# Optimization experiments

Measured on AMD Instinct MI355X. Metric: run time of the kernel, lower is better.

The kernel has to match this reference:

```python
import jax, jax.numpy as jnp
import numpy as np

N_NODES = 100000
HID = 128
N_EDGES = 600000


def sage_conv(h, src, dst, Wl, bl, Wr, n_nodes):
    # PyG SAGEConv (mean aggr): out = lin_l(mean_{j->i} h_j) + lin_r(h_i)
    msgs = h[src]                                               # [E, d] gather
    agg = jax.ops.segment_sum(msgs, dst, num_segments=n_nodes)  # [N, d]
    cnt = jax.ops.segment_sum(jnp.ones((src.shape[0], 1), h.dtype), dst,
                              num_segments=n_nodes)             # [N, 1]
    mean = agg / jnp.maximum(cnt, 1.0)                          # isolated nodes -> 0
    return mean @ Wl.T + bl + h @ Wr.T


def setup_inputs() -> dict:
    key = jax.random.key(0)
    ks = jax.random.split(key, 8)
    scale = 1.0 / np.sqrt(HID)
    x = jnp.arange(N_NODES, dtype=jnp.int64) if jax.config.jax_enable_x64 else jnp.arange(N_NODES, dtype=jnp.int32)
    edge_index = jax.random.randint(ks[0], (2, N_EDGES), 0, N_NODES)
    emb = jax.random.normal(ks[1], (N_NODES, HID), dtype=jnp.float32) * scale
    Wl1 = jax.random.normal(ks[2], (HID, HID), dtype=jnp.float32) * scale
    bl1 = jnp.zeros((HID,), jnp.float32)
    Wr1 = jax.random.normal(ks[3], (HID, HID), dtype=jnp.float32) * scale
    Wl2 = jax.random.normal(ks[4], (HID, HID), dtype=jnp.float32) * scale
    bl2 = jnp.zeros((HID,), jnp.float32)
    Wr2 = jax.random.normal(ks[5], (HID, HID), dtype=jnp.float32) * scale
    return {"x": x, "edge_index": edge_index, "emb": emb,
            "Wl1": Wl1, "bl1": bl1, "Wr1": Wr1,
            "Wl2": Wl2, "bl2": bl2, "Wr2": Wr2}


def reference(x, edge_index, emb, Wl1, bl1, Wr1, Wl2, bl2, Wr2):
    src, dst = edge_index[0], edge_index[1]
    n = emb.shape[0]
    h = emb[x]                                          # embedding lookup [N, d]
    h = jax.nn.relu(sage_conv(h, src, dst, Wl1, bl1, Wr1, n))  # dropout = eval identity
    h = jax.nn.relu(sage_conv(h, src, dst, Wl2, bl2, Wr2, n))
    return h
```

## Files before the change

kernel.cpp:

```cpp
#include <hip/hip_runtime.h>

#define HID 128

typedef unsigned short ushort_t;
typedef unsigned int uint_t;
typedef float f32x4 __attribute__((ext_vector_type(4)));
typedef short s16x8 __attribute__((ext_vector_type(8)));

__device__ __forceinline__ ushort_t f2bf(float f) {
  uint_t u = __float_as_uint(f);
  uint_t r = (u + 0x7FFFu + ((u >> 16) & 1u)) >> 16;
  return (ushort_t)r;
}
__device__ __forceinline__ float bfLo(uint_t v) { return __uint_as_float(v << 16); }
__device__ __forceinline__ float bfHi(uint_t v) { return __uint_as_float(v & 0xFFFF0000u); }

__global__ __launch_bounds__(256) void prep_kernel(
    const float* __restrict__ emb, const int* __restrict__ x,
    ushort_t* __restrict__ hb, int N,
    const float* __restrict__ Wl1, const float* __restrict__ Wr1,
    const float* __restrict__ Wl2, const float* __restrict__ Wr2,
    ushort_t* __restrict__ wsw,
    const int* __restrict__ dst, int* __restrict__ deg, int E) {
  int tid = blockIdx.x * 256 + threadIdx.x;
  const int halfN = (N + 1) >> 1;
  int gthreads = halfN * 16;
  if (tid < gthreads) {
    int r0 = tid >> 4, j = (tid & 15) * 8;
    int r1 = r0 + halfN;
    int s0 = x[r0];
    int s1 = (r1 < N) ? x[r1] : s0;
    const float* src0 = &emb[(size_t)s0 * HID + j];
    const float* src1 = &emb[(size_t)s1 * HID + j];
    float4 a0 = *(const float4*)src0;
    float4 a1 = *(const float4*)(src0 + 4);
    float4 b0 = *(const float4*)src1;
    float4 b1 = *(const float4*)(src1 + 4);
    uint4 p;
    p.x = (uint_t)f2bf(a0.x) | ((uint_t)f2bf(a0.y) << 16);
    p.y = (uint_t)f2bf(a0.z) | ((uint_t)f2bf(a0.w) << 16);
    p.z = (uint_t)f2bf(a1.x) | ((uint_t)f2bf(a1.y) << 16);
    p.w = (uint_t)f2bf(a1.z) | ((uint_t)f2bf(a1.w) << 16);
    *(uint4*)&hb[(size_t)r0 * HID + j] = p;
    if (r1 < N) {
      uint4 q;
      q.x = (uint_t)f2bf(b0.x) | ((uint_t)f2bf(b0.y) << 16);
      q.y = (uint_t)f2bf(b0.z) | ((uint_t)f2bf(b0.w) << 16);
      q.z = (uint_t)f2bf(b1.x) | ((uint_t)f2bf(b1.y) << 16);
      q.w = (uint_t)f2bf(b1.z) | ((uint_t)f2bf(b1.w) << 16);
      *(uint4*)&hb[(size_t)r1 * HID + j] = q;
    }
    return;
  }
  tid -= gthreads;
  if (tid < 65536) {
    const float* srcs[4] = {Wl1, Wr1, Wl2, Wr2};
    int m = tid >> 14, idx = tid & 16383;
    int j = idx & 7;
    int lane = (idx >> 3) & 63;
    int nt = (idx >> 9) & 7;
    int ks = (idx >> 12) & 3;
    int row = nt * 16 + (lane & 15);
    int col = ks * 32 + (lane >> 4) * 8 + j;
    wsw[tid] = f2bf(srcs[m][row * HID + col]);
    return;
  }
  tid -= 65536;
  if (tid < E) atomicAdd(&deg[dst[tid]], 1);
}

__global__ __launch_bounds__(256) void scan1_kernel(
    const int* __restrict__ deg, int* __restrict__ offsets,
    int* __restrict__ sums, int N) {
  __shared__ int s[256];
  int b = blockIdx.x, t = threadIdx.x;
  int base = b * 1024 + t * 4;
  int v0 = 0, v1 = 0, v2 = 0, v3 = 0;
  if (base + 0 < N) v0 = deg[base + 0];
  if (base + 1 < N) v1 = deg[base + 1];
  if (base + 2 < N) v2 = deg[base + 2];
  if (base + 3 < N) v3 = deg[base + 3];
  int mySum = v0 + v1 + v2 + v3;
  s[t] = mySum;
  __syncthreads();
  for (int off = 1; off < 256; off <<= 1) {
    int v = (t >= off) ? s[t - off] : 0;
    __syncthreads();
    s[t] += v;
    __syncthreads();
  }
  int excl = s[t] - mySum;
  if (t == 255) sums[b] = s[255];
  if (base + 0 < N) offsets[base + 0] = excl;
  if (base + 1 < N) offsets[base + 1] = excl + v0;
  if (base + 2 < N) offsets[base + 2] = excl + v0 + v1;
  if (base + 3 < N) offsets[base + 3] = excl + v0 + v1 + v2;
}

__global__ __launch_bounds__(256) void scan3_kernel(
    int* __restrict__ offsets, const int* __restrict__ sums,
    int* __restrict__ cursor, int N, int E, int nb) {
  __shared__ int red[256];
  int t = threadIdx.x;
  int chunk = (blockIdx.x * 256) >> 10;
  red[t] = (t < chunk) ? sums[t] : 0;
  __syncthreads();
  for (int off = 128; off > 0; off >>= 1) {
    if (t < off) red[t] += red[t + off];
    __syncthreads();
  }
  int prefix = red[0];
  int i = blockIdx.x * 256 + t;
  if (i < N) {
    int v = offsets[i] + prefix;
    offsets[i] = v;
    cursor[i] = v;
  } else if (i == N) {
    offsets[N] = E;
  }
}

__global__ __launch_bounds__(256) void fill_kernel(
    const int* __restrict__ src, const int* __restrict__ dst,
    int* __restrict__ cursor, int* __restrict__ csr, int E) {
  int e = blockIdx.x * 256 + threadIdx.x;
  if (e >= E) return;
  int d = dst[e];
  int pos = atomicAdd(&cursor[d], 1);
  csr[pos] = src[e];
}

__global__ __launch_bounds__(256) void aggregate_kernel(
    const ushort_t* __restrict__ hb, const int* __restrict__ offsets,
    const int* __restrict__ csr, ushort_t* __restrict__ meanb, int N) {
  int t = threadIdx.x;
  int node = blockIdx.x * 16 + (t >> 4);
  if (node >= N) return;
  int l15 = t & 15;
  int o0 = offsets[node], o1 = offsets[node + 1];

  float acc[8];
#pragma unroll
  for (int i = 0; i < 8; i++) acc[i] = 0.f;

  int e = o0;
  for (; e + 3 < o1; e += 4) {
    int s0 = csr[e], s1 = csr[e + 1], s2 = csr[e + 2], s3 = csr[e + 3];
    uint4 v0 = *(const uint4*)&hb[(size_t)s0 * HID + l15 * 8];
    uint4 v1 = *(const uint4*)&hb[(size_t)s1 * HID + l15 * 8];
    uint4 v2 = *(const uint4*)&hb[(size_t)s2 * HID + l15 * 8];
    uint4 v3 = *(const uint4*)&hb[(size_t)s3 * HID + l15 * 8];
    acc[0] += (bfLo(v0.x) + bfLo(v1.x)) + (bfLo(v2.x) + bfLo(v3.x));
    acc[1] += (bfHi(v0.x) + bfHi(v1.x)) + (bfHi(v2.x) + bfHi(v3.x));
    acc[2] += (bfLo(v0.y) + bfLo(v1.y)) + (bfLo(v2.y) + bfLo(v3.y));
    acc[3] += (bfHi(v0.y) + bfHi(v1.y)) + (bfHi(v2.y) + bfHi(v3.y));
    acc[4] += (bfLo(v0.z) + bfLo(v1.z)) + (bfLo(v2.z) + bfLo(v3.z));
    acc[5] += (bfHi(v0.z) + bfHi(v1.z)) + (bfHi(v2.z) + bfHi(v3.z));
    acc[6] += (bfLo(v0.w) + bfLo(v1.w)) + (bfLo(v2.w) + bfLo(v3.w));
    acc[7] += (bfHi(v0.w) + bfHi(v1.w)) + (bfHi(v2.w) + bfHi(v3.w));
  }
  if (e + 1 < o1) {
    int s0 = csr[e], s1 = csr[e + 1];
    uint4 v0 = *(const uint4*)&hb[(size_t)s0 * HID + l15 * 8];
    uint4 v1 = *(const uint4*)&hb[(size_t)s1 * HID + l15 * 8];
    acc[0] += bfLo(v0.x) + bfLo(v1.x);
    acc[1] += bfHi(v0.x) + bfHi(v1.x);
    acc[2] += bfLo(v0.y) + bfLo(v1.y);
    acc[3] += bfHi(v0.y) + bfHi(v1.y);
    acc[4] += bfLo(v0.z) + bfLo(v1.z);
    acc[5] += bfHi(v0.z) + bfHi(v1.z);
    acc[6] += bfLo(v0.w) + bfLo(v1.w);
    acc[7] += bfHi(v0.w) + bfHi(v1.w);
    e += 2;
  }
  if (e < o1) {
    int s0 = csr[e];
    uint4 v0 = *(const uint4*)&hb[(size_t)s0 * HID + l15 * 8];
    acc[0] += bfLo(v0.x); acc[1] += bfHi(v0.x);
    acc[2] += bfLo(v0.y); acc[3] += bfHi(v0.y);
    acc[4] += bfLo(v0.z); acc[5] += bfHi(v0.z);
    acc[6] += bfLo(v0.w); acc[7] += bfHi(v0.w);
  }

  int d = o1 - o0;
  float inv = 1.0f / (float)(d > 1 ? d : 1);
  uint4 p;
  p.x = (uint_t)f2bf(acc[0] * inv) | ((uint_t)f2bf(acc[1] * inv) << 16);
  p.y = (uint_t)f2bf(acc[2] * inv) | ((uint_t)f2bf(acc[3] * inv) << 16);
  p.z = (uint_t)f2bf(acc[4] * inv) | ((uint_t)f2bf(acc[5] * inv) << 16);
  p.w = (uint_t)f2bf(acc[6] * inv) | ((uint_t)f2bf(acc[7] * inv) << 16);
  *(uint4*)&meanb[(size_t)node * HID + l15 * 8] = p;
}

__global__ __launch_bounds__(256) void mfma_gemm_kernel(
    const ushort_t* __restrict__ meanb, const ushort_t* __restrict__ hb,
    const ushort_t* __restrict__ WlS, const ushort_t* __restrict__ WrS,
    const float* __restrict__ bias, float* __restrict__ outF,
    ushort_t* __restrict__ outB, int N, int outIsBf16) {
  __shared__ ushort_t ws[32768];
  const int t = threadIdx.x;
  const int wave = t >> 6;
  const int lane = t & 63;
  const int rowBase = (blockIdx.x * 4 + wave) * 32;
  const int l15 = lane & 15;
  const int quad = lane >> 4;
  const int kq = quad * 8;
  const bool active = rowBase < N;

  int r0 = rowBase + l15;       if (r0 >= N) r0 = N - 1;
  int r1 = rowBase + 16 + l15;  if (r1 >= N) r1 = N - 1;

  s16x8 a[2][2][4];
  if (active) {
#pragma unroll
    for (int ks = 0; ks < 4; ks++) {
      a[0][0][ks] = *(const s16x8*)&meanb[(size_t)r0 * HID + ks * 32 + kq];
      a[0][1][ks] = *(const s16x8*)&meanb[(size_t)r1 * HID + ks * 32 + kq];
      a[1][0][ks] = *(const s16x8*)&hb[(size_t)r0 * HID + ks * 32 + kq];
      a[1][1][ks] = *(const s16x8*)&hb[(size_t)r1 * HID + ks * 32 + kq];
    }
  }

#pragma unroll
  for (int it = 0; it < 8; it++) {
    int o = (it * 256 + t) * 8;
    *(s16x8*)&ws[o] = *(const s16x8*)&WlS[o];
    *(s16x8*)&ws[16384 + o] = *(const s16x8*)&WrS[o];
  }
  __syncthreads();

  if (active) {
    f32x4 acc[2][8];
#pragma unroll
    for (int mt = 0; mt < 2; mt++)
#pragma unroll
      for (int nt = 0; nt < 8; nt++) acc[mt][nt] = (f32x4){0.f, 0.f, 0.f, 0.f};

#pragma unroll
    for (int half = 0; half < 2; half++) {
      const int hbase = half * 16384;
#pragma unroll
      for (int ks = 0; ks < 4; ks++)
#pragma unroll
        for (int nt = 0; nt < 8; nt++) {
          s16x8 b = *(const s16x8*)&ws[hbase + ((ks * 8 + nt) * 64 + lane) * 8];
          acc[0][nt] = __builtin_amdgcn_mfma_f32_16x16x32_bf16(a[half][0][ks], b, acc[0][nt], 0, 0, 0);
          acc[1][nt] = __builtin_amdgcn_mfma_f32_16x16x32_bf16(a[half][1][ks], b, acc[1][nt], 0, 0, 0);
        }
    }

#pragma unroll
    for (int mt = 0; mt < 2; mt++) {
#pragma unroll
      for (int nt = 0; nt < 8; nt++) {
        int col = nt * 16 + l15;
        float bv = bias[col];
#pragma unroll
        for (int r = 0; r < 4; r++) {
          int row = rowBase + mt * 16 + quad * 4 + r;
          if (row < N) {
            float v = fmaxf(acc[mt][nt][r] + bv, 0.f);
            if (outIsBf16) outB[(size_t)row * HID + col] = f2bf(v);
            else           outF[(size_t)row * HID + col] = v;
          }
        }
      }
    }
  }
}

extern "C" void kernel_launch(void* const* d_in, const int* in_sizes, int n_in,
                              void* d_out, int out_size, void* d_ws, size_t ws_size,
                              hipStream_t stream) {
  const int* x = (const int*)d_in[0];
  const int* ei = (const int*)d_in[1];
  const float* emb = (const float*)d_in[2];
  const float* Wl1 = (const float*)d_in[3];
  const float* bl1 = (const float*)d_in[4];
  const float* Wr1 = (const float*)d_in[5];
  const float* Wl2 = (const float*)d_in[6];
  const float* bl2 = (const float*)d_in[7];
  const float* Wr2 = (const float*)d_in[8];
  float* out = (float*)d_out;

  const int N = in_sizes[0];
  const int E = in_sizes[1] / 2;
  const int* srcI = ei;
  const int* dstI = ei + E;

  char* p = (char*)d_ws;
  ushort_t* hb = (ushort_t*)p;    p += (size_t)N * HID * sizeof(ushort_t);
  ushort_t* meanb = (ushort_t*)p; p += (size_t)N * HID * sizeof(ushort_t);
  ushort_t* wb = (ushort_t*)p;    p += (size_t)4 * 16384 * sizeof(ushort_t);
  int* deg = (int*)p;             p += (size_t)((N + 3) & ~3) * sizeof(int);
  int* offsets = (int*)p;         p += (size_t)((N + 4) & ~3) * sizeof(int);
  int* cursor = (int*)p;          p += (size_t)((N + 3) & ~3) * sizeof(int);
  int* csr = (int*)p;             p += (size_t)((E + 3) & ~3) * sizeof(int);
  int* sums = (int*)p;            p += 256 * sizeof(int);

  ushort_t* Wlb1 = wb;
  ushort_t* Wrb1 = wb + 16384;
  ushort_t* Wlb2 = wb + 32768;
  ushort_t* Wrb2 = wb + 49152;

  const int nScanBlocks = (N + 1023) / 1024;
  const int eBlocks = (E + 255) / 256;
  const int gemmBlocks = (N + 127) / 128;
  const int aggBlocks = (N + 15) / 16;
  const int halfN = (N + 1) / 2;
  const int prepBlocks = (halfN * 16 + 65536 + E + 255) / 256;

  hipMemsetAsync(deg, 0, (size_t)N * sizeof(int), stream);
  prep_kernel<<<prepBlocks, 256, 0, stream>>>(emb, x, hb, N,
                                              Wl1, Wr1, Wl2, Wr2, wb,
                                              dstI, deg, E);
  scan1_kernel<<<nScanBlocks, 256, 0, stream>>>(deg, offsets, sums, N);
  scan3_kernel<<<(N + 256) / 256, 256, 0, stream>>>(offsets, sums, cursor,
                                                    N, E, nScanBlocks);
  fill_kernel<<<eBlocks, 256, 0, stream>>>(srcI, dstI, cursor, csr, E);

  aggregate_kernel<<<aggBlocks, 256, 0, stream>>>(hb, offsets, csr, meanb, N);
  mfma_gemm_kernel<<<gemmBlocks, 256, 0, stream>>>(meanb, hb, Wlb1, Wrb1, bl1,
                                                   nullptr, hb, N, 1);

  aggregate_kernel<<<aggBlocks, 256, 0, stream>>>(hb, offsets, csr, meanb, N);
  mfma_gemm_kernel<<<gemmBlocks, 256, 0, stream>>>(meanb, hb, Wlb2, Wrb2, bl2,
                                                   out, nullptr, N, 0);
}
```

Measured before the change: 293.6 us.

## Fuse mean aggregation with MFMA GEMM per layer via LDS mean tile

Merges the aggregate and GEMM kernels into one per-layer kernel. Each block gathers neighbour means for its 128 rows into a padded LDS tile and feeds them straight to the MFMA loop, removing the global round trip of the mean buffer and one launch per layer. Weights are now staged in quarter-size LDS chunks with extra barriers so the mean tile fits, and ping-pong hb buffers avoid read/write hazards. The prep kernel also handles four embedding rows per thread instead of two.

```diff
diff --git a/kernel.cpp b/kernel.cpp
--- a/kernel.cpp
+++ b/kernel.cpp
@@ -1,6 +1,7 @@
 #include <hip/hip_runtime.h>
 
 #define HID 128
+#define MEAN_STRIDE 136
 
 typedef unsigned short ushort_t;
 typedef unsigned int uint_t;
@@ -14,6 +15,15 @@
 }
 __device__ __forceinline__ float bfLo(uint_t v) { return __uint_as_float(v << 16); }
 __device__ __forceinline__ float bfHi(uint_t v) { return __uint_as_float(v & 0xFFFF0000u); }
+
+__device__ __forceinline__ uint4 pack8(const float4& lo, const float4& hi) {
+  uint4 p;
+  p.x = (uint_t)f2bf(lo.x) | ((uint_t)f2bf(lo.y) << 16);
+  p.y = (uint_t)f2bf(lo.z) | ((uint_t)f2bf(lo.w) << 16);
+  p.z = (uint_t)f2bf(hi.x) | ((uint_t)f2bf(hi.y) << 16);
+  p.w = (uint_t)f2bf(hi.z) | ((uint_t)f2bf(hi.w) << 16);
+  return p;
+}
 
 __global__ __launch_bounds__(256) void prep_kernel(
     const float* __restrict__ emb, const int* __restrict__ x,
@@ -23,33 +33,27 @@
     ushort_t* __restrict__ wsw,
     const int* __restrict__ dst, int* __restrict__ deg, int E) {
   int tid = blockIdx.x * 256 + threadIdx.x;
-  const int halfN = (N + 1) >> 1;
-  int gthreads = halfN * 16;
+  const int qN = (N + 3) >> 2;
+  int gthreads = qN * 16;
   if (tid < gthreads) {
     int r0 = tid >> 4, j = (tid & 15) * 8;
-    int r1 = r0 + halfN;
+    int r1 = r0 + qN, r2 = r0 + 2 * qN, r3 = r0 + 3 * qN;
     int s0 = x[r0];
     int s1 = (r1 < N) ? x[r1] : s0;
-    const float* src0 = &emb[(size_t)s0 * HID + j];
-    const float* src1 = &emb[(size_t)s1 * HID + j];
-    float4 a0 = *(const float4*)src0;
-    float4 a1 = *(const float4*)(src0 + 4);
-    float4 b0 = *(const float4*)src1;
-    float4 b1 = *(const float4*)(src1 + 4);
-    uint4 p;
-    p.x = (uint_t)f2bf(a0.x) | ((uint_t)f2bf(a0.y) << 16);
-    p.y = (uint_t)f2bf(a0.z) | ((uint_t)f2bf(a0.w) << 16);
-    p.z = (uint_t)f2bf(a1.x) | ((uint_t)f2bf(a1.y) << 16);
-    p.w = (uint_t)f2bf(a1.z) | ((uint_t)f2bf(a1.w) << 16);
-    *(uint4*)&hb[(size_t)r0 * HID + j] = p;
-    if (r1 < N) {
-      uint4 q;
-      q.x = (uint_t)f2bf(b0.x) | ((uint_t)f2bf(b0.y) << 16);
-      q.y = (uint_t)f2bf(b0.z) | ((uint_t)f2bf(b0.w) << 16);
-      q.z = (uint_t)f2bf(b1.x) | ((uint_t)f2bf(b1.y) << 16);
-      q.w = (uint_t)f2bf(b1.z) | ((uint_t)f2bf(b1.w) << 16);
-      *(uint4*)&hb[(size_t)r1 * HID + j] = q;
-    }
+    int s2 = (r2 < N) ? x[r2] : s0;
+    int s3 = (r3 < N) ? x[r3] : s0;
+    const float* p0 = &emb[(size_t)s0 * HID + j];
+    const float* p1 = &emb[(size_t)s1 * HID + j];
+    const float* p2 = &emb[(size_t)s2 * HID + j];
+    const float* p3 = &emb[(size_t)s3 * HID + j];
+    float4 a0 = *(const float4*)p0, a1 = *(const float4*)(p0 + 4);
+    float4 b0 = *(const float4*)p1, b1 = *(const float4*)(p1 + 4);
+    float4 c0 = *(const float4*)p2, c1 = *(const float4*)(p2 + 4);
+    float4 d0 = *(const float4*)p3, d1 = *(const float4*)(p3 + 4);
+    *(uint4*)&hb[(size_t)r0 * HID + j] = pack8(a0, a1);
+    if (r1 < N) *(uint4*)&hb[(size_t)r1 * HID + j] = pack8(b0, b1);
+    if (r2 < N) *(uint4*)&hb[(size_t)r2 * HID + j] = pack8(c0, c1);
+    if (r3 < N) *(uint4*)&hb[(size_t)r3 * HID + j] = pack8(d0, d1);
     return;
   }
   tid -= gthreads;
@@ -130,125 +134,150 @@
   csr[pos] = src[e];
 }
 
-__global__ __launch_bounds__(256) void aggregate_kernel(
-    const ushort_t* __restrict__ hb, const int* __restrict__ offsets,
-    const int* __restrict__ csr, ushort_t* __restrict__ meanb, int N) {
-  int t = threadIdx.x;
-  int node = blockIdx.x * 16 + (t >> 4);
-  if (node >= N) return;
-  int l15 = t & 15;
-  int o0 = offsets[node], o1 = offsets[node + 1];
-
-  float acc[8];
-#pragma unroll
-  for (int i = 0; i < 8; i++) acc[i] = 0.f;
-
-  int e = o0;
-  for (; e + 3 < o1; e += 4) {
-    int s0 = csr[e], s1 = csr[e + 1], s2 = csr[e + 2], s3 = csr[e + 3];
-    uint4 v0 = *(const uint4*)&hb[(size_t)s0 * HID + l15 * 8];
-    uint4 v1 = *(const uint4*)&hb[(size_t)s1 * HID + l15 * 8];
-    uint4 v2 = *(const uint4*)&hb[(size_t)s2 * HID + l15 * 8];
-    uint4 v3 = *(const uint4*)&hb[(size_t)s3 * HID + l15 * 8];
-    acc[0] += (bfLo(v0.x) + bfLo(v1.x)) + (bfLo(v2.x) + bfLo(v3.x));
-    acc[1] += (bfHi(v0.x) + bfHi(v1.x)) + (bfHi(v2.x) + bfHi(v3.x));
-    acc[2] += (bfLo(v0.y) + bfLo(v1.y)) + (bfLo(v2.y) + bfLo(v3.y));
-    acc[3] += (bfHi(v0.y) + bfHi(v1.y)) + (bfHi(v2.y) + bfHi(v3.y));
-    acc[4] += (bfLo(v0.z) + bfLo(v1.z)) + (bfLo(v2.z) + bfLo(v3.z));
-    acc[5] += (bfHi(v0.z) + bfHi(v1.z)) + (bfHi(v2.z) + bfHi(v3.z));
-    acc[6] += (bfLo(v0.w) + bfLo(v1.w)) + (bfLo(v2.w) + bfLo(v3.w));
-    acc[7] += (bfHi(v0.w) + bfHi(v1.w)) + (bfHi(v2.w) + bfHi(v3.w));
-  }
-  if (e + 1 < o1) {
-    int s0 = csr[e], s1 = csr[e + 1];
-    uint4 v0 = *(const uint4*)&hb[(size_t)s0 * HID + l15 * 8];
-    uint4 v1 = *(const uint4*)&hb[(size_t)s1 * HID + l15 * 8];
-    acc[0] += bfLo(v0.x) + bfLo(v1.x);
-    acc[1] += bfHi(v0.x) + bfHi(v1.x);
-    acc[2] += bfLo(v0.y) + bfLo(v1.y);
-    acc[3] += bfHi(v0.y) + bfHi(v1.y);
-    acc[4] += bfLo(v0.z) + bfLo(v1.z);
-    acc[5] += bfHi(v0.z) + bfHi(v1.z);
-    acc[6] += bfLo(v0.w) + bfLo(v1.w);
-    acc[7] += bfHi(v0.w) + bfHi(v1.w);
-    e += 2;
-  }
-  if (e < o1) {
-    int s0 = csr[e];
-    uint4 v0 = *(const uint4*)&hb[(size_t)s0 * HID + l15 * 8];
-    acc[0] += bfLo(v0.x); acc[1] += bfHi(v0.x);
-    acc[2] += bfLo(v0.y); acc[3] += bfHi(v0.y);
-    acc[4] += bfLo(v0.z); acc[5] += bfHi(v0.z);
-    acc[6] += bfLo(v0.w); acc[7] += bfHi(v0.w);
-  }
-
-  int d = o1 - o0;
-  float inv = 1.0f / (float)(d > 1 ? d : 1);
-  uint4 p;
-  p.x = (uint_t)f2bf(acc[0] * inv) | ((uint_t)f2bf(acc[1] * inv) << 16);
-  p.y = (uint_t)f2bf(acc[2] * inv) | ((uint_t)f2bf(acc[3] * inv) << 16);
-  p.z = (uint_t)f2bf(acc[4] * inv) | ((uint_t)f2bf(acc[5] * inv) << 16);
-  p.w = (uint_t)f2bf(acc[6] * inv) | ((uint_t)f2bf(acc[7] * inv) << 16);
-  *(uint4*)&meanb[(size_t)node * HID + l15 * 8] = p;
-}
-
-__global__ __launch_bounds__(256) void mfma_gemm_kernel(
-    const ushort_t* __restrict__ meanb, const ushort_t* __restrict__ hb,
+__global__ __launch_bounds__(256, 3) void fused_layer_kernel(
+    const ushort_t* __restrict__ hbIn,
+    const int* __restrict__ offsets, const int* __restrict__ csr,
     const ushort_t* __restrict__ WlS, const ushort_t* __restrict__ WrS,
-    const float* __restrict__ bias, float* __restrict__ outF,
-    ushort_t* __restrict__ outB, int N, int outIsBf16) {
-  __shared__ ushort_t ws[32768];
+    const float* __restrict__ bias,
+    float* __restrict__ outF, ushort_t* __restrict__ outB,
+    int N, int outIsBf16) {
+  __shared__ ushort_t lmean[128 * MEAN_STRIDE];
+  __shared__ ushort_t ws[8192];
   const int t = threadIdx.x;
+  const int lane = t & 63;
   const int wave = t >> 6;
-  const int lane = t & 63;
-  const int rowBase = (blockIdx.x * 4 + wave) * 32;
   const int l15 = lane & 15;
   const int quad = lane >> 4;
   const int kq = quad * 8;
-  const bool active = rowBase < N;
-
-  int r0 = rowBase + l15;       if (r0 >= N) r0 = N - 1;
-  int r1 = rowBase + 16 + l15;  if (r1 >= N) r1 = N - 1;
-
-  s16x8 a[2][2][4];
+  const int blockRow = blockIdx.x * 128;
+  const int waveRow = blockRow + wave * 32;
+  const bool active = waveRow < N;
+
+  int r0 = waveRow + l15;      if (r0 >= N) r0 = N - 1;
+  int r1 = waveRow + 16 + l15; if (r1 >= N) r1 = N - 1;
+  s16x8 ah0[4], ah1[4];
+#pragma unroll
+  for (int ks = 0; ks < 4; ks++) {
+    ah0[ks] = *(const s16x8*)&hbIn[(size_t)r0 * HID + ks * 32 + kq];
+    ah1[ks] = *(const s16x8*)&hbIn[(size_t)r1 * HID + ks * 32 + kq];
+  }
+
+  const int qw = t >> 4;
+#pragma unroll 1
+  for (int i = 0; i < 8; i++) {
+    int rl = qw * 8 + i;
+    int node = blockRow + rl;
+    uint4 p;
+    p.x = p.y = p.z = p.w = 0u;
+    if (node < N) {
+      int o0 = offsets[node], o1 = offsets[node + 1];
+      float acc[8];
+#pragma unroll
+      for (int q = 0; q < 8; q++) acc[q] = 0.f;
+      int e = o0;
+      for (; e + 3 < o1; e += 4) {
+        int s0 = csr[e], s1 = csr[e + 1], s2 = csr[e + 2], s3 = csr[e + 3];
+        uint4 v0 = *(const uint4*)&hbIn[(size_t)s0 * HID + l15 * 8];
+        uint4 v1 = *(const uint4*)&hbIn[(size_t)s1 * HID + l15 * 8];
+        uint4 v2 = *(const uint4*)&hbIn[(size_t)s2 * HID + l15 * 8];
+        uint4 v3 = *(const uint4*)&hbIn[(size_t)s3 * HID + l15 * 8];
+        acc[0] += (bfLo(v0.x) + bfLo(v1.x)) + (bfLo(v2.x) + bfLo(v3.x));
+        acc[1] += (bfHi(v0.x) + bfHi(v1.x)) + (bfHi(v2.x) + bfHi(v3.x));
+        acc[2] += (bfLo(v0.y) + bfLo(v1.y)) + (bfLo(v2.y) + bfLo(v3.y));
+        acc[3] += (bfHi(v0.y) + bfHi(v1.y)) + (bfHi(v2.y) + bfHi(v3.y));
+        acc[4] += (bfLo(v0.z) + bfLo(v1.z)) + (bfLo(v2.z) + bfLo(v3.z));
+        acc[5] += (bfHi(v0.z) + bfHi(v1.z)) + (bfHi(v2.z) + bfHi(v3.z));
+        acc[6] += (bfLo(v0.w) + bfLo(v1.w)) + (bfLo(v2.w) + bfLo(v3.w));
+        acc[7] += (bfHi(v0.w) + bfHi(v1.w)) + (bfHi(v2.w) + bfHi(v3.w));
+      }
+      if (e + 1 < o1) {
+        int s0 = csr[e], s1 = csr[e + 1];
+        uint4 v0 = *(const uint4*)&hbIn[(size_t)s0 * HID + l15 * 8];
+        uint4 v1 = *(const uint4*)&hbIn[(size_t)s1 * HID + l15 * 8];
+        acc[0] += bfLo(v0.x) + bfLo(v1.x);
+        acc[1] += bfHi(v0.x) + bfHi(v1.x);
+        acc[2] += bfLo(v0.y) + bfLo(v1.y);
+        acc[3] += bfHi(v0.y) + bfHi(v1.y);
+        acc[4] += bfLo(v0.z) + bfLo(v1.z);
+        acc[5] += bfHi(v0.z) + bfHi(v1.z);
+        acc[6] += bfLo(v0.w) + bfLo(v1.w);
+        acc[7] += bfHi(v0.w) + bfHi(v1.w);
+        e += 2;
+      }
+      if (e < o1) {
+        int s0 = csr[e];
+        uint4 v0 = *(const uint4*)&hbIn[(size_t)s0 * HID + l15 * 8];
+        acc[0] += bfLo(v0.x); acc[1] += bfHi(v0.x);
+        acc[2] += bfLo(v0.y); acc[3] += bfHi(v0.y);
+        acc[4] += bfLo(v0.z); acc[5] += bfHi(v0.z);
+        acc[6] += bfLo(v0.w); acc[7] += bfHi(v0.w);
+      }
+      int d = o1 - o0;
+      float inv = 1.0f / (float)(d > 1 ? d : 1);
+      p.x = (uint_t)f2bf(acc[0] * inv) | ((uint_t)f2bf(acc[1] * inv) << 16);
+      p.y = (uint_t)f2bf(acc[2] * inv) | ((uint_t)f2bf(acc[3] * inv) << 16);
+      p.z = (uint_t)f2bf(acc[4] * inv) | ((uint_t)f2bf(acc[5] * inv) << 16);
+      p.w = (uint_t)f2bf(acc[6] * inv) | ((uint_t)f2bf(acc[7] * inv) << 16);
+    }
+    *(uint4*)&lmean[rl * MEAN_STRIDE + l15 * 8] = p;
+  }
+  __syncthreads();
+
+  f32x4 acc[2][8];
+#pragma unroll
+  for (int mt = 0; mt < 2; mt++)
+#pragma unroll
+    for (int nt = 0; nt < 8; nt++) acc[mt][nt] = (f32x4){0.f, 0.f, 0.f, 0.f};
+
+#pragma unroll
+  for (int kp = 0; kp < 2; kp++) {
+#pragma unroll
+    for (int it = 0; it < 4; it++) {
+      int o = (it * 256 + t) * 8;
+      *(s16x8*)&ws[o] = *(const s16x8*)&WlS[kp * 8192 + o];
+    }
+    __syncthreads();
+    if (active) {
+#pragma unroll
+      for (int ks2 = 0; ks2 < 2; ks2++) {
+        int ksg = kp * 2 + ks2;
+        s16x8 a0 = *(const s16x8*)&lmean[(wave * 32 + l15) * MEAN_STRIDE + ksg * 32 + kq];
+        s16x8 a1 = *(const s16x8*)&lmean[(wave * 32 + 16 + l15) * MEAN_STRIDE + ksg * 32 + kq];
+#pragma unroll
+        for (int nt = 0; nt < 8; nt++) {
+          s16x8 b = *(const s16x8*)&ws[((ks2 * 8 + nt) * 64 + lane) * 8];
+          acc[0][nt] = __builtin_amdgcn_mfma_f32_16x16x32_bf16(a0, b, acc[0][nt], 0, 0, 0);
+          acc[1][nt] = __builtin_amdgcn_mfma_f32_16x16x32_bf16(a1, b, acc[1][nt], 0, 0, 0);
+        }
+      }
+    }
+    __syncthreads();
+  }
+
+#pragma unroll
+  for (int kp = 0; kp < 2; kp++) {
+#pragma unroll
+    for (int it = 0; it < 4; it++) {
+      int o = (it * 256 + t) * 8;
+      *(s16x8*)&ws[o] = *(const s16x8*)&WrS[kp * 8192 + o];
+    }
+    __syncthreads();
+    if (active) {
+#pragma unroll
+      for (int ks2 = 0; ks2 < 2; ks2++) {
+        int ksg = kp * 2 + ks2;
+#pragma unroll
+        for (int nt = 0; nt < 8; nt++) {
+          s16x8 b = *(const s16x8*)&ws[((ks2 * 8 + nt) * 64 + lane) * 8];
+          acc[0][nt] = __builtin_amdgcn_mfma_f32_16x16x32_bf16(ah0[ksg], b, acc[0][nt], 0, 0, 0);
+          acc[1][nt] = __builtin_amdgcn_mfma_f32_16x16x32_bf16(ah1[ksg], b, acc[1][nt], 0, 0, 0);
+        }
+      }
+    }
+    __syncthreads();
+  }
+
   if (active) {
-#pragma unroll
-    for (int ks = 0; ks < 4; ks++) {
-      a[0][0][ks] = *(const s16x8*)&meanb[(size_t)r0 * HID + ks * 32 + kq];
-      a[0][1][ks] = *(const s16x8*)&meanb[(size_t)r1 * HID + ks * 32 + kq];
-      a[1][0][ks] = *(const s16x8*)&hb[(size_t)r0 * HID + ks * 32 + kq];
-      a[1][1][ks] = *(const s16x8*)&hb[(size_t)r1 * HID + ks * 32 + kq];
-    }
-  }
-
-#pragma unroll
-  for (int it = 0; it < 8; it++) {
-    int o = (it * 256 + t) * 8;
-    *(s16x8*)&ws[o] = *(const s16x8*)&WlS[o];
-    *(s16x8*)&ws[16384 + o] = *(const s16x8*)&WrS[o];
-  }
-  __syncthreads();
-
-  if (active) {
-    f32x4 acc[2][8];
-#pragma unroll
-    for (int mt = 0; mt < 2; mt++)
-#pragma unroll
-      for (int nt = 0; nt < 8; nt++) acc[mt][nt] = (f32x4){0.f, 0.f, 0.f, 0.f};
-
-#pragma unroll
-    for (int half = 0; half < 2; half++) {
-      const int hbase = half * 16384;
-#pragma unroll
-      for (int ks = 0; ks < 4; ks++)
-#pragma unroll
-        for (int nt = 0; nt < 8; nt++) {
-          s16x8 b = *(const s16x8*)&ws[hbase + ((ks * 8 + nt) * 64 + lane) * 8];
-          acc[0][nt] = __builtin_amdgcn_mfma_f32_16x16x32_bf16(a[half][0][ks], b, acc[0][nt], 0, 0, 0);
-          acc[1][nt] = __builtin_amdgcn_mfma_f32_16x16x32_bf16(a[half][1][ks], b, acc[1][nt], 0, 0, 0);
-        }
-    }
-
 #pragma unroll
     for (int mt = 0; mt < 2; mt++) {
 #pragma unroll
@@ -257,7 +286,7 @@
         float bv = bias[col];
 #pragma unroll
         for (int r = 0; r < 4; r++) {
-          int row = rowBase + mt * 16 + quad * 4 + r;
+          int row = waveRow + mt * 16 + quad * 4 + r;
           if (row < N) {
             float v = fmaxf(acc[mt][nt][r] + bv, 0.f);
             if (outIsBf16) outB[(size_t)row * HID + col] = f2bf(v);
@@ -290,7 +319,7 @@
 
   char* p = (char*)d_ws;
   ushort_t* hb = (ushort_t*)p;    p += (size_t)N * HID * sizeof(ushort_t);
-  ushort_t* meanb = (ushort_t*)p; p += (size_t)N * HID * sizeof(ushort_t);
+  ushort_t* hb2 = (ushort_t*)p;   p += (size_t)N * HID * sizeof(ushort_t);
   ushort_t* wb = (ushort_t*)p;    p += (size_t)4 * 16384 * sizeof(ushort_t);
   int* deg = (int*)p;             p += (size_t)((N + 3) & ~3) * sizeof(int);
   int* offsets = (int*)p;         p += (size_t)((N + 4) & ~3) * sizeof(int);
@@ -306,9 +335,8 @@
   const int nScanBlocks = (N + 1023) / 1024;
   const int eBlocks = (E + 255) / 256;
   const int gemmBlocks = (N + 127) / 128;
-  const int aggBlocks = (N + 15) / 16;
-  const int halfN = (N + 1) / 2;
-  const int prepBlocks = (halfN * 16 + 65536 + E + 255) / 256;
+  const int qN = (N + 3) / 4;
+  const int prepBlocks = (qN * 16 + 65536 + E + 255) / 256;
 
   hipMemsetAsync(deg, 0, (size_t)N * sizeof(int), stream);
   prep_kernel<<<prepBlocks, 256, 0, stream>>>(emb, x, hb, N,
@@ -319,11 +347,10 @@
                                                     N, E, nScanBlocks);
   fill_kernel<<<eBlocks, 256, 0, stream>>>(srcI, dstI, cursor, csr, E);
 
-  aggregate_kernel<<<aggBlocks, 256, 0, stream>>>(hb, offsets, csr, meanb, N);
-  mfma_gemm_kernel<<<gemmBlocks, 256, 0, stream>>>(meanb, hb, Wlb1, Wrb1, bl1,
-                                                   nullptr, hb, N, 1);
-
-  aggregate_kernel<<<aggBlocks, 256, 0, stream>>>(hb, offsets, csr, meanb, N);
-  mfma_gemm_kernel<<<gemmBlocks, 256, 0, stream>>>(meanb, hb, Wlb2, Wrb2, bl2,
-                                                   out, nullptr, N, 0);
-}
+  fused_layer_kernel<<<gemmBlocks, 256, 0, stream>>>(hb, offsets, csr,
+                                                     Wlb1, Wrb1, bl1,
+                                                     nullptr, hb2, N, 1);
+  fused_layer_kernel<<<gemmBlocks, 256, 0, stream>>>(hb2, offsets, csr,
+                                                     Wlb2, Wrb2, bl2,
+                                                     out, nullptr, N, 0);
+}
```

New measurement: 336.4 us. 14.6% more time.
